# Optimization experiments

Measured on AMD Instinct MI355X. Metric: run time of the kernel, lower is better.

Reference implementation:

```python
import jax, jax.numpy as jnp
import numpy as np

B, T, E, H = 8, 2048, 1024, 128

def setup_inputs() -> dict:
    key = jax.random.key(0)
    k1, k2, k3, k4 = jax.random.split(key, 4)
    s = 0.02
    return {
        "x":  jax.random.normal(k1, (B, T, E), dtype=jnp.float32),
        "Wq": jax.random.normal(k2, (E, H), dtype=jnp.float32) * s,
        "Wk": jax.random.normal(k3, (E, H), dtype=jnp.float32) * s,
        "Wv": jax.random.normal(k4, (E, H), dtype=jnp.float32) * s,
    }

def reference(x, Wq, Wk, Wv):
    # q,k,v: [B,T,H]
    q = jnp.einsum("bte,eh->bth", x, Wq)
    k = jnp.einsum("bte,eh->bth", x, Wk)
    v = jnp.einsum("bte,eh->bth", x, Wv)
    scale = jnp.asarray(q.shape[-1], q.dtype) ** -0.5
    wei = jnp.einsum("bqh,bkh->bqk", q, k) * scale  # [B,T,T]
    causal = jnp.tril(jnp.ones((wei.shape[1], wei.shape[2]), dtype=bool))
    wei = jnp.where(causal, wei, jnp.asarray(-jnp.inf, wei.dtype))
    wei = jax.nn.softmax(wei, axis=-1)
    # dropout_prob = 0.0 -> identity
    return jnp.einsum("bqk,bkh->bqh", wei, v)
```

## Files before the change

kernel.cpp:

```cpp
#include <hip/hip_runtime.h>

#define BB 8
#define TT 2048
#define EE 1024
#define HH 128

typedef __bf16 bf16;
typedef __attribute__((ext_vector_type(8))) __bf16 bf16x8;
typedef __attribute__((ext_vector_type(4))) __bf16 bf16x4;
typedef __attribute__((ext_vector_type(4))) float f32x4;
typedef __attribute__((ext_vector_type(16))) float f32x16;

__device__ __host__ inline int qb_off(int qb) {
  int h = qb >> 1;
  return qb + h * (h - 1) + ((qb & 1) ? h : 0);
}
#define NSLAB 72

__device__ inline void gload_lds16(const bf16* g, bf16* l) {
  __builtin_amdgcn_global_load_lds((const __attribute__((address_space(1))) unsigned int*)g,
                                   (__attribute__((address_space(3))) unsigned int*)l,
                                   16, 0, 0);
}

__global__ __launch_bounds__(256) void prep_kernel(const float* __restrict__ x,
                                                   bf16* __restrict__ xb,
                                                   const float* __restrict__ wq,
                                                   const float* __restrict__ wk,
                                                   const float* __restrict__ wv,
                                                   bf16* __restrict__ wt) {
  __shared__ float tile[64][65];
  const int bid = blockIdx.x;
  if (bid < 4096) {
    const size_t base = (size_t)bid * 4096 + threadIdx.x * 4;
#pragma unroll
    for (int j = 0; j < 4; ++j) {
      size_t idx = base + j * 1024;
      f32x4 xv = *(const f32x4*)(x + idx);
      bf16x4 xo;
#pragma unroll
      for (int i = 0; i < 4; ++i) xo[i] = (bf16)xv[i];
      *(bf16x4*)(xb + idx) = xo;
    }
  } else {
    const int id = bid - 4096;
    const int z = id >> 5;
    const int h0 = ((id >> 4) & 1) * 64;
    const int k0 = (id & 15) * 64;
    const float* w = (z == 0) ? wq : ((z == 1) ? wk : wv);
    const int c = threadIdx.x & 63;
    const int r0 = threadIdx.x >> 6;
#pragma unroll
    for (int i = 0; i < 16; ++i) {
      int tt = r0 + i * 4;
      tile[tt][c] = w[(size_t)(k0 + tt) * HH + h0 + c];
    }
    __syncthreads();
#pragma unroll
    for (int i = 0; i < 16; ++i) {
      int hh = r0 + i * 4;
      wt[((size_t)(z * HH + h0 + hh)) * EE + k0 + c] = (bf16)tile[c][hh];
    }
  }
}

__global__ __launch_bounds__(256) void gemm_kernel(const bf16* __restrict__ xb,
                                                   const bf16* __restrict__ wt,
                                                   bf16* __restrict__ q,
                                                   bf16* __restrict__ k,
                                                   bf16* __restrict__ vt) {
  __shared__ bf16 As[2][64 * 32];
  __shared__ bf16 Bs[2][96 * 32];
  const int tid = threadIdx.x;
  const int lane = tid & 63;
  const int wave = tid >> 6;
  const int l16 = lane & 15;
  const int quad = lane >> 4;
  const int wm = wave & 1;
  const int wn = wave >> 1;
  const int bm = blockIdx.x;
  const int ntile = blockIdx.y;

  const int trow = tid >> 2;
  const int tsub = (tid & 3) * 8;
  const bf16* gA = xb + (size_t)(bm * 64 + trow) * EE + tsub;
  const bf16* gB = wt + (size_t)(ntile * 96 + trow) * EE + tsub;

  f32x4 acc[2][3];
#pragma unroll
  for (int rg = 0; rg < 2; ++rg)
#pragma unroll
    for (int nt = 0; nt < 3; ++nt) acc[rg][nt] = f32x4{0.f, 0.f, 0.f, 0.f};

  auto stage = [&](int bufi, int ks) {
    gload_lds16(gA + ks * 32, &As[bufi][wave * 512]);
    gload_lds16(gB + ks * 32, &Bs[bufi][wave * 512]);
    if (tid < 128)
      gload_lds16(gB + (size_t)64 * EE + ks * 32, &Bs[bufi][2048 + wave * 512]);
  };

  stage(0, 0);
  __syncthreads();

  int buf = 0;
  for (int ks = 0; ks < EE / 32; ++ks) {
    if (ks < EE / 32 - 1) stage(buf ^ 1, ks + 1);

    bf16x8 af[2], bf_[3];
#pragma unroll
    for (int rg = 0; rg < 2; ++rg)
      af[rg] = *(const bf16x8*)&As[buf][(wm * 32 + rg * 16 + l16) * 32 + quad * 8];
#pragma unroll
    for (int nt = 0; nt < 3; ++nt)
      bf_[nt] = *(const bf16x8*)&Bs[buf][(wn * 48 + nt * 16 + l16) * 32 + quad * 8];
#pragma unroll
    for (int rg = 0; rg < 2; ++rg)
#pragma unroll
      for (int nt = 0; nt < 3; ++nt)
        acc[rg][nt] = __builtin_amdgcn_mfma_f32_16x16x32_bf16(af[rg], bf_[nt], acc[rg][nt], 0, 0, 0);

    __syncthreads();
    buf ^= 1;
  }

#pragma unroll
  for (int rg = 0; rg < 2; ++rg)
#pragma unroll
    for (int nt = 0; nt < 3; ++nt) {
      int col = ntile * 96 + wn * 48 + nt * 16 + l16;
      int z = col >> 7;
      int n = col & 127;
      int row0 = bm * 64 + wm * 32 + rg * 16 + quad * 4;
      if (z == 2) {
        int bb = row0 >> 11;
        int t0 = row0 & (TT - 1);
        bf16x4 pkv;
#pragma unroll
        for (int r = 0; r < 4; ++r) pkv[r] = (bf16)acc[rg][nt][r];
        *(bf16x4*)&vt[((size_t)(bb * HH + n)) * TT + t0] = pkv;
      } else {
        bf16* op = (z == 0) ? q : k;
#pragma unroll
        for (int r = 0; r < 4; ++r)
          op[(size_t)(row0 + r) * HH + n] = (bf16)acc[rg][nt][r];
      }
    }
}

__device__ __forceinline__ unsigned pk2(float a, float b) {
  union { __bf16 h[2]; unsigned u; } x;
  x.h[0] = (__bf16)a;
  x.h[1] = (__bf16)b;
  return x.u;
}

__device__ __forceinline__ void plswap(unsigned& a, unsigned& b) {
  asm volatile("v_permlane32_swap_b32 %0, %1" : "+v"(a), "+v"(b));
}

__global__ __launch_bounds__(256, 2) void flash_kernel(const bf16* __restrict__ q,
                                                       const bf16* __restrict__ k,
                                                       const bf16* __restrict__ vt,
                                                       bf16* __restrict__ opart,
                                                       float* __restrict__ lpart) {
  __shared__ bf16 Ks[2][64 * 128];
  __shared__ bf16 Vs[2][128 * 64];

  const int b = blockIdx.x & 7;
  int j = (NSLAB - 1) - (blockIdx.x >> 3);
  int qb = 0, ns = 1;
  while (j >= ns) { j -= ns; ++qb; ns = ((2 * qb + 1) >> 2) + 1; }
  const int s = j;
  const int kt0 = s * 4;
  const int kt1 = min(kt0 + 3, 2 * qb + 1);

  const int tid = threadIdx.x;
  const int lane = tid & 63;
  const int wave = tid >> 6;
  const int l32 = lane & 31;
  const int hi = lane >> 5;
  const int qrow = qb * 128 + wave * 32 + l32;
  const int kdiag = qb * 4 + wave;

  bf16x8 qf[8];
  {
    const bf16* qp = q + (size_t)(b * TT + qrow) * HH + hi * 8;
#pragma unroll
    for (int h16 = 0; h16 < 8; ++h16) qf[h16] = *(const bf16x8*)(qp + h16 * 16);
  }

  f32x16 O[4];
#pragma unroll
  for (int ht = 0; ht < 4; ++ht)
#pragma unroll
    for (int r = 0; r < 16; ++r) O[ht][r] = 0.f;
  float L = 0.f;

  const int krow_s = tid >> 4;
  const int kchk_s = (tid & 15) ^ (krow_s & 7);
  const int vrow_s = tid >> 3;
  const int vchk_s = (tid & 7) ^ (vrow_s & 7);
  const bf16* kg = k + (size_t)b * TT * HH;
  const bf16* vg = vt + (size_t)b * HH * TT;

  auto stageKV = [&](int bufi, int kt) {
#pragma unroll
    for (int i = 0; i < 4; ++i)
      gload_lds16(kg + (size_t)(kt * 64 + i * 16 + krow_s) * HH + kchk_s * 8,
                  &Ks[bufi][(i * 256 + wave * 64) * 8]);
#pragma unroll
    for (int i = 0; i < 4; ++i)
      gload_lds16(vg + (size_t)(i * 32 + vrow_s) * TT + kt * 64 + vchk_s * 8,
                  &Vs[bufi][(i * 256 + wave * 64) * 8]);
  };

  const int kxor = (l32 & 7) << 3;
  const float c_ = 0.12753257680406733f;

  stageKV(0, kt0);
  __syncthreads();

  int buf = 0;
  for (int kt = kt0; kt <= kt1; ++kt) {
    if (kt < kt1) stageKV(buf ^ 1, kt + 1);

#pragma unroll
    for (int khalf = 0; khalf < 2; ++khalf) {
      const int k32 = kt * 2 + khalf;
      if (k32 <= kdiag) {
        const bf16* kls = &Ks[buf][(khalf * 32 + l32) * 128];
        bf16x8 kf[8];
#pragma unroll
        for (int h16 = 0; h16 < 8; ++h16)
          kf[h16] = *(const bf16x8*)&kls[(h16 * 16 + hi * 8) ^ kxor];

        f32x16 S;
#pragma unroll
        for (int r = 0; r < 16; ++r) S[r] = 0.f;
#pragma unroll
        for (int h16 = 0; h16 < 8; ++h16)
          S = __builtin_amdgcn_mfma_f32_32x32x16_bf16(kf[h16], qf[h16], S, 0, 0, 0);

        float p[16];
        if (k32 == kdiag) {
          const int kkb = k32 * 32 + 4 * hi;
#pragma unroll
          for (int r = 0; r < 16; ++r) {
            int kk = kkb + (r & 3) + 8 * (r >> 2);
            p[r] = (kk <= qrow) ? exp2f(S[r] * c_) : 0.f;
          }
        } else {
#pragma unroll
          for (int r = 0; r < 16; ++r) p[r] = exp2f(S[r] * c_);
        }
        L += (((p[0] + p[1]) + (p[2] + p[3])) + ((p[4] + p[5]) + (p[6] + p[7]))) +
             (((p[8] + p[9]) + (p[10] + p[11])) + ((p[12] + p[13]) + (p[14] + p[15])));

#pragma unroll
        for (int s16 = 0; s16 < 2; ++s16) {
          unsigned w0 = pk2(p[s16 * 8 + 0], p[s16 * 8 + 1]);
          unsigned w1 = pk2(p[s16 * 8 + 2], p[s16 * 8 + 3]);
          unsigned w2 = pk2(p[s16 * 8 + 4], p[s16 * 8 + 5]);
          unsigned w3 = pk2(p[s16 * 8 + 6], p[s16 * 8 + 7]);
          plswap(w0, w2);
          plswap(w1, w3);
          union { unsigned u[4]; bf16x8 v; } af;
          af.u[0] = w0;
          af.u[1] = w1;
          af.u[2] = w2;
          af.u[3] = w3;
          bf16x8 vf[4];
#pragma unroll
          for (int ht = 0; ht < 4; ++ht)
            vf[ht] = *(const bf16x8*)&Vs[buf][(l32 + 32 * ht) * 64 +
                                             ((khalf * 32 + s16 * 16 + hi * 8) ^ kxor)];
#pragma unroll
          for (int ht = 0; ht < 4; ++ht)
            O[ht] = __builtin_amdgcn_mfma_f32_32x32x16_bf16(af.v, vf[ht], O[ht], 0, 0, 0);
        }
      }
    }
    __syncthreads();
    buf ^= 1;
  }

  L += __shfl_xor(L, 32, 64);

  const size_t slab = (size_t)(b * NSLAB + qb_off(qb) + s);
  bf16* op = opart + slab * (128 * 128) + (size_t)wave * 32 * 128;
#pragma unroll
  for (int ht = 0; ht < 4; ++ht)
#pragma unroll
    for (int r = 0; r < 16; ++r) {
      int qr = (r & 3) + 8 * (r >> 2) + 4 * hi;
      op[qr * 128 + ht * 32 + l32] = (bf16)O[ht][r];
    }
  if (hi == 0) lpart[slab * 128 + wave * 32 + l32] = L;
}

__global__ __launch_bounds__(128) void combine_kernel(const bf16* __restrict__ opart,
                                                      const float* __restrict__ lpart,
                                                      float* __restrict__ out) {
  const int b = blockIdx.x;
  const int qt16 = blockIdx.y;
  const int half = blockIdx.z;
  const int row = threadIdx.x >> 3;
  const int colo = (threadIdx.x & 7) * 8 + half * 64;
  const int qb = qt16 >> 3;
  const int srow = (qt16 & 7) * 16 + row;
  const int ns = ((2 * qb + 1) >> 2) + 1;
  const size_t slab0 = (size_t)(b * NSLAB + qb_off(qb));

  float acc[8];
#pragma unroll
  for (int j = 0; j < 8; ++j) acc[j] = 0.f;
  float L = 0.f;

  int s = 0;
  for (; s + 4 <= ns; s += 4) {
    float l0 = lpart[(slab0 + s + 0) * 128 + srow];
    float l1 = lpart[(slab0 + s + 1) * 128 + srow];
    float l2 = lpart[(slab0 + s + 2) * 128 + srow];
    float l3 = lpart[(slab0 + s + 3) * 128 + srow];
    bf16x8 v0 = *(const bf16x8*)(opart + (slab0 + s + 0) * (128 * 128) + srow * 128 + colo);
    bf16x8 v1 = *(const bf16x8*)(opart + (slab0 + s + 1) * (128 * 128) + srow * 128 + colo);
    bf16x8 v2 = *(const bf16x8*)(opart + (slab0 + s + 2) * (128 * 128) + srow * 128 + colo);
    bf16x8 v3 = *(const bf16x8*)(opart + (slab0 + s + 3) * (128 * 128) + srow * 128 + colo);
    L += (l0 + l1) + (l2 + l3);
#pragma unroll
    for (int j = 0; j < 8; ++j)
      acc[j] += ((float)v0[j] + (float)v1[j]) + ((float)v2[j] + (float)v3[j]);
  }
  for (; s < ns; ++s) {
    L += lpart[(slab0 + s) * 128 + srow];
    bf16x8 ov = *(const bf16x8*)(opart + (slab0 + s) * (128 * 128) + srow * 128 + colo);
#pragma unroll
    for (int j = 0; j < 8; ++j) acc[j] += (float)ov[j];
  }
  float invL = 1.f / L;
  float* o = out + ((size_t)(b * TT + qt16 * 16 + row)) * HH + colo;
  f32x4 o0, o1;
#pragma unroll
  for (int j = 0; j < 4; ++j) { o0[j] = acc[j] * invL; o1[j] = acc[j + 4] * invL; }
  *(f32x4*)o = o0;
  *(f32x4*)(o + 4) = o1;
}

extern "C" void kernel_launch(void* const* d_in, const int* in_sizes, int n_in,
                              void* d_out, int out_size, void* d_ws, size_t ws_size,
                              hipStream_t stream) {
  const float* x = (const float*)d_in[0];
  const float* wq = (const float*)d_in[1];
  const float* wk = (const float*)d_in[2];
  const float* wv = (const float*)d_in[3];
  float* out = (float*)d_out;

  char* ws = (char*)d_ws;
  const size_t NE = (size_t)BB * TT * HH;
  bf16* wt = (bf16*)ws;
  bf16* xb = (bf16*)(ws + (1 << 20));
  bf16* q = (bf16*)(ws + (33 << 20));
  bf16* k = q + NE;
  bf16* vt = k + NE;
  bf16* opart = xb;
  float* lpart = (float*)(opart + (size_t)(BB * NSLAB) * 128 * 128);

  prep_kernel<<<dim3(4192), 256, 0, stream>>>(x, xb, wq, wk, wv, wt);
  gemm_kernel<<<dim3(256, 4), 256, 0, stream>>>(xb, wt, q, k, vt);
  flash_kernel<<<dim3(576), 256, 0, stream>>>(q, k, vt, opart, lpart);
  combine_kernel<<<dim3(8, 128, 2), 128, 0, stream>>>(opart, lpart, out);
}
```

Baseline: 154.3 us.

## Fuse x fp32-to-bf16 conversion into QKV GEMM and widen tile to all outputs

Removes the separate pass that converts x to bf16 into a workspace. The GEMM now loads fp32 x directly, converts it in registers and writes it into LDS, using a 512-thread block that computes all 384 QKV columns per 64-row tile so x is read only once. The weight transpose becomes its own small kernel. Separately, the flash kernel raises wave priority around its MFMA sequences. The trade-off is a larger LDS footprint, fewer GEMM blocks (256), and A-tile loads going through registers instead of direct global-to-LDS copies.

```diff
diff --git a/kernel.cpp b/kernel.cpp
--- a/kernel.cpp
+++ b/kernel.cpp
@@ -23,102 +23,100 @@
                                    16, 0, 0);
 }
 
-__global__ __launch_bounds__(256) void prep_kernel(const float* __restrict__ x,
-                                                   bf16* __restrict__ xb,
-                                                   const float* __restrict__ wq,
-                                                   const float* __restrict__ wk,
-                                                   const float* __restrict__ wv,
-                                                   bf16* __restrict__ wt) {
+__global__ __launch_bounds__(256) void wt_kernel(const float* __restrict__ wq,
+                                                 const float* __restrict__ wk,
+                                                 const float* __restrict__ wv,
+                                                 bf16* __restrict__ wt) {
   __shared__ float tile[64][65];
-  const int bid = blockIdx.x;
-  if (bid < 4096) {
-    const size_t base = (size_t)bid * 4096 + threadIdx.x * 4;
-#pragma unroll
-    for (int j = 0; j < 4; ++j) {
-      size_t idx = base + j * 1024;
-      f32x4 xv = *(const f32x4*)(x + idx);
-      bf16x4 xo;
-#pragma unroll
-      for (int i = 0; i < 4; ++i) xo[i] = (bf16)xv[i];
-      *(bf16x4*)(xb + idx) = xo;
-    }
-  } else {
-    const int id = bid - 4096;
-    const int z = id >> 5;
-    const int h0 = ((id >> 4) & 1) * 64;
-    const int k0 = (id & 15) * 64;
-    const float* w = (z == 0) ? wq : ((z == 1) ? wk : wv);
-    const int c = threadIdx.x & 63;
-    const int r0 = threadIdx.x >> 6;
-#pragma unroll
-    for (int i = 0; i < 16; ++i) {
-      int tt = r0 + i * 4;
-      tile[tt][c] = w[(size_t)(k0 + tt) * HH + h0 + c];
-    }
-    __syncthreads();
-#pragma unroll
-    for (int i = 0; i < 16; ++i) {
-      int hh = r0 + i * 4;
-      wt[((size_t)(z * HH + h0 + hh)) * EE + k0 + c] = (bf16)tile[c][hh];
-    }
-  }
-}
-
-__global__ __launch_bounds__(256) void gemm_kernel(const bf16* __restrict__ xb,
+  const int z = blockIdx.z;
+  const float* w = (z == 0) ? wq : ((z == 1) ? wk : wv);
+  const int k0 = blockIdx.x * 64;
+  const int h0 = blockIdx.y * 64;
+  const int c = threadIdx.x & 63;
+  const int r0 = threadIdx.x >> 6;
+#pragma unroll
+  for (int i = 0; i < 16; ++i) {
+    int tt = r0 + i * 4;
+    tile[tt][c] = w[(size_t)(k0 + tt) * HH + h0 + c];
+  }
+  __syncthreads();
+#pragma unroll
+  for (int i = 0; i < 16; ++i) {
+    int hh = r0 + i * 4;
+    wt[((size_t)(z * HH + h0 + hh)) * EE + k0 + c] = (bf16)tile[c][hh];
+  }
+}
+
+__global__ __launch_bounds__(512) void gemm_kernel(const float* __restrict__ x,
                                                    const bf16* __restrict__ wt,
                                                    bf16* __restrict__ q,
                                                    bf16* __restrict__ k,
                                                    bf16* __restrict__ vt) {
   __shared__ bf16 As[2][64 * 32];
-  __shared__ bf16 Bs[2][96 * 32];
+  __shared__ bf16 Bs[2][384 * 32];
   const int tid = threadIdx.x;
   const int lane = tid & 63;
   const int wave = tid >> 6;
   const int l16 = lane & 15;
   const int quad = lane >> 4;
-  const int wm = wave & 1;
-  const int wn = wave >> 1;
+  const int wm = wave >> 2;
+  const int wn = wave & 3;
   const int bm = blockIdx.x;
-  const int ntile = blockIdx.y;
-
-  const int trow = tid >> 2;
-  const int tsub = (tid & 3) * 8;
-  const bf16* gA = xb + (size_t)(bm * 64 + trow) * EE + tsub;
-  const bf16* gB = wt + (size_t)(ntile * 96 + trow) * EE + tsub;
-
-  f32x4 acc[2][3];
+
+  const bf16* gB = wt + (size_t)(tid >> 2) * EE + (tid & 3) * 8;
+  const int arow = tid >> 3;
+  const int akc = (tid & 7) * 4;
+  const float* gA = x + (size_t)(bm * 64 + arow) * EE + akc;
+
+  f32x4 acc[2][6];
 #pragma unroll
   for (int rg = 0; rg < 2; ++rg)
 #pragma unroll
-    for (int nt = 0; nt < 3; ++nt) acc[rg][nt] = f32x4{0.f, 0.f, 0.f, 0.f};
-
-  auto stage = [&](int bufi, int ks) {
-    gload_lds16(gA + ks * 32, &As[bufi][wave * 512]);
-    gload_lds16(gB + ks * 32, &Bs[bufi][wave * 512]);
-    if (tid < 128)
-      gload_lds16(gB + (size_t)64 * EE + ks * 32, &Bs[bufi][2048 + wave * 512]);
+    for (int nt = 0; nt < 6; ++nt) acc[rg][nt] = f32x4{0.f, 0.f, 0.f, 0.f};
+
+  auto stageB = [&](int bufi, int ks) {
+#pragma unroll
+    for (int i = 0; i < 3; ++i)
+      gload_lds16(gB + (size_t)i * 128 * EE + ks * 32, &Bs[bufi][i * 4096 + wave * 512]);
   };
 
-  stage(0, 0);
+  {
+    f32x4 av = *(const f32x4*)gA;
+    stageB(0, 0);
+    bf16x4 ab;
+#pragma unroll
+    for (int jj = 0; jj < 4; ++jj) ab[jj] = (bf16)av[jj];
+    *(bf16x4*)&As[0][arow * 32 + akc] = ab;
+  }
   __syncthreads();
 
   int buf = 0;
   for (int ks = 0; ks < EE / 32; ++ks) {
-    if (ks < EE / 32 - 1) stage(buf ^ 1, ks + 1);
-
-    bf16x8 af[2], bf_[3];
+    f32x4 av;
+    if (ks < EE / 32 - 1) {
+      av = *(const f32x4*)(gA + (ks + 1) * 32);
+      stageB(buf ^ 1, ks + 1);
+    }
+
+    bf16x8 af[2], bf_[6];
 #pragma unroll
     for (int rg = 0; rg < 2; ++rg)
       af[rg] = *(const bf16x8*)&As[buf][(wm * 32 + rg * 16 + l16) * 32 + quad * 8];
 #pragma unroll
-    for (int nt = 0; nt < 3; ++nt)
-      bf_[nt] = *(const bf16x8*)&Bs[buf][(wn * 48 + nt * 16 + l16) * 32 + quad * 8];
+    for (int nt = 0; nt < 6; ++nt)
+      bf_[nt] = *(const bf16x8*)&Bs[buf][(wn * 96 + nt * 16 + l16) * 32 + quad * 8];
 #pragma unroll
     for (int rg = 0; rg < 2; ++rg)
 #pragma unroll
-      for (int nt = 0; nt < 3; ++nt)
+      for (int nt = 0; nt < 6; ++nt)
         acc[rg][nt] = __builtin_amdgcn_mfma_f32_16x16x32_bf16(af[rg], bf_[nt], acc[rg][nt], 0, 0, 0);
 
+    if (ks < EE / 32 - 1) {
+      bf16x4 ab;
+#pragma unroll
+      for (int jj = 0; jj < 4; ++jj) ab[jj] = (bf16)av[jj];
+      *(bf16x4*)&As[buf ^ 1][arow * 32 + akc] = ab;
+    }
     __syncthreads();
     buf ^= 1;
   }
@@ -126,8 +124,8 @@
 #pragma unroll
   for (int rg = 0; rg < 2; ++rg)
 #pragma unroll
-    for (int nt = 0; nt < 3; ++nt) {
-      int col = ntile * 96 + wn * 48 + nt * 16 + l16;
+    for (int nt = 0; nt < 6; ++nt) {
+      int col = wn * 96 + nt * 16 + l16;
       int z = col >> 7;
       int n = col & 127;
       int row0 = bm * 64 + wm * 32 + rg * 16 + quad * 4;
@@ -237,9 +235,11 @@
         f32x16 S;
 #pragma unroll
         for (int r = 0; r < 16; ++r) S[r] = 0.f;
+        __builtin_amdgcn_s_setprio(1);
 #pragma unroll
         for (int h16 = 0; h16 < 8; ++h16)
           S = __builtin_amdgcn_mfma_f32_32x32x16_bf16(kf[h16], qf[h16], S, 0, 0, 0);
+        __builtin_amdgcn_s_setprio(0);
 
         float p[16];
         if (k32 == kdiag) {
@@ -274,9 +274,11 @@
           for (int ht = 0; ht < 4; ++ht)
             vf[ht] = *(const bf16x8*)&Vs[buf][(l32 + 32 * ht) * 64 +
                                              ((khalf * 32 + s16 * 16 + hi * 8) ^ kxor)];
+          __builtin_amdgcn_s_setprio(1);
 #pragma unroll
           for (int ht = 0; ht < 4; ++ht)
             O[ht] = __builtin_amdgcn_mfma_f32_32x32x16_bf16(af.v, vf[ht], O[ht], 0, 0, 0);
+          __builtin_amdgcn_s_setprio(0);
         }
       }
     }
@@ -358,15 +360,14 @@
   char* ws = (char*)d_ws;
   const size_t NE = (size_t)BB * TT * HH;
   bf16* wt = (bf16*)ws;
-  bf16* xb = (bf16*)(ws + (1 << 20));
-  bf16* q = (bf16*)(ws + (33 << 20));
+  bf16* q = (bf16*)(ws + (1 << 20));
   bf16* k = q + NE;
   bf16* vt = k + NE;
-  bf16* opart = xb;
+  bf16* opart = (bf16*)(ws + (16 << 20));
   float* lpart = (float*)(opart + (size_t)(BB * NSLAB) * 128 * 128);
 
-  prep_kernel<<<dim3(4192), 256, 0, stream>>>(x, xb, wq, wk, wv, wt);
-  gemm_kernel<<<dim3(256, 4), 256, 0, stream>>>(xb, wt, q, k, vt);
+  wt_kernel<<<dim3(16, 2, 3), 256, 0, stream>>>(wq, wk, wv, wt);
+  gemm_kernel<<<dim3(256), 512, 0, stream>>>(x, wt, q, k, vt);
   flash_kernel<<<dim3(576), 256, 0, stream>>>(q, k, vt, opart, lpart);
   combine_kernel<<<dim3(8, 128, 2), 128, 0, stream>>>(opart, lpart, out);
 }
```

After: 162.2 us. 1.05x slower.
